# Kernel tuning notes

Hardware: AMD Instinct MI355X
Metric: run time of the kernel (lower is better)

Reference implementation:

```python
import jax, jax.numpy as jnp
import numpy as np

B, H, W, C = 4, 64, 64, 64
GROUPS = 32
EPS = 1e-3  # keras GroupNormalization default


def setup_inputs() -> dict:
    key = jax.random.key(0)
    ks = jax.random.split(key, 6)
    s = 1.0 / np.sqrt(C)
    return {
        'x': jax.random.normal(ks[0], (B, H, W, C), dtype=jnp.float32),
        'gamma': jnp.ones((C,), jnp.float32),
        'beta': jnp.zeros((C,), jnp.float32),
        'wq': jax.random.uniform(ks[1], (C, C), jnp.float32, -s, s),
        'bq': jnp.zeros((C,), jnp.float32),
        'wk': jax.random.uniform(ks[2], (C, C), jnp.float32, -s, s),
        'bk': jnp.zeros((C,), jnp.float32),
        'wv': jax.random.uniform(ks[3], (C, C), jnp.float32, -s, s),
        'bv': jnp.zeros((C,), jnp.float32),
        'wo': jnp.zeros((C, C), jnp.float32),  # init_scale=0.0 -> ~zero init
        'bo': jnp.zeros((C,), jnp.float32),
    }


def group_norm(x, gamma, beta):
    b, h, w, c = x.shape
    xg = x.reshape(b, h, w, GROUPS, c // GROUPS)
    mean = jnp.mean(xg, axis=(1, 2, 4), keepdims=True)
    var = jnp.var(xg, axis=(1, 2, 4), keepdims=True)
    xn = ((xg - mean) * jax.lax.rsqrt(var + EPS)).reshape(b, h, w, c)
    return xn * gamma + beta


def reference(x, gamma, beta, wq, bq, wk, bk, wv, bv, wo, bo):
    b, h, w, c = x.shape
    hn = group_norm(x, gamma, beta)
    # 1x1 convs == per-pixel dense layers
    q = jnp.einsum('bhwc,cd->bhwd', hn, wq) + bq
    k = jnp.einsum('bhwc,cd->bhwd', hn, wk) + bk
    v = jnp.einsum('bhwc,cd->bhwd', hn, wv) + bv
    # full spatial attention scores [B,H,W,H,W]
    scores = jnp.einsum('bhwc,bHWc->bhwHW', q, k) * (float(c) ** -0.5)
    attn = jax.nn.softmax(scores.reshape(b, h, w, h * w), axis=-1)
    attn = attn.reshape(b, h, w, h, w)
    o = jnp.einsum('bhwHW,bHWc->bhwc', attn, v)
    o = jnp.einsum('bhwc,cd->bhwd', o, wo) + bo
    return x + o
```

## Files before the change

kernel.cpp:

```cpp
#include <hip/hip_runtime.h>
#include <math.h>

#define BB 4
#define HH 64
#define WW 64
#define CC 64
#define NN (HH*WW)
#define NPIX (BB*NN)
#define EPS 1e-3f
#define QBLK 32
#define KSPLIT 8
#define NQT32 (NPIX/QBLK)
#define NCHK ((NN/KSPLIT)/64)

using bf16x8 = __attribute__((ext_vector_type(8))) short;
using f32x4  = __attribute__((ext_vector_type(4))) float;
using f32x16 = __attribute__((ext_vector_type(16))) float;

__device__ inline unsigned short bf16bits(float f) {
    union { float f; unsigned u; } a; a.f = f;
    unsigned r = a.u + 0x7fffu + ((a.u >> 16) & 1u);
    return (unsigned short)(r >> 16);
}
__device__ inline unsigned packbf(float lo, float hi) {
    return (unsigned)bf16bits(lo) | ((unsigned)bf16bits(hi) << 16);
}
__device__ inline unsigned cvtpk(float lo, float hi) {
    unsigned r;
    asm("v_cvt_pk_bf16_f32 %0, %1, %2" : "=v"(r) : "v"(lo), "v"(hi));
    return r;
}
#define PSWAP(a, b) asm("v_permlane32_swap_b32 %0, %1" : "+v"(a), "+v"(b))

__device__ __forceinline__ float exp2g(float x) {
    float r;
    asm("v_exp_f32 %0, %1" : "=v"(r) : "v"(x));
    return r;
}

#define QSCALE 0.18033688011112042f

__global__ __launch_bounds__(256) void gn_wt(const float* __restrict__ x,
                                             float* __restrict__ part,
                                             const float* __restrict__ wq,
                                             const float* __restrict__ wk,
                                             const float* __restrict__ wv,
                                             const float* __restrict__ wo,
                                             short* __restrict__ wfrag) {
    int t = threadIdx.x;
    if (blockIdx.x < 256) {
        int c = t & 63, rr = t >> 6;
        int p0 = blockIdx.x * 64;
        float s = 0.f, s2 = 0.f;
        #pragma unroll
        for (int k = 0; k < 16; ++k) {
            float v = x[(size_t)(p0 + rr + 4 * k) * CC + c];
            s += v; s2 += v * v;
        }
        __shared__ float sA[256], sB[256];
        sA[t] = s; sB[t] = s2;
        __syncthreads();
        if (t < 64) {
            float fs  = sA[t] + sA[64 + t] + sA[128 + t] + sA[192 + t];
            float fs2 = sB[t] + sB[64 + t] + sB[128 + t] + sB[192 + t];
            part[blockIdx.x * 128 + t]      = fs;
            part[blockIdx.x * 128 + 64 + t] = fs2;
        }
    } else {
        const float* mats[3] = {wq, wk, wv};
        int i0 = (blockIdx.x - 256) * 256 + t;
        for (int e = i0; e < 12288; e += 16 * 256) {
            int m = e >> 12;
            int r = e & 4095;
            int dt = r >> 10, h = (r >> 9) & 1, lane = (r >> 3) & 63, j = r & 7;
            int g = lane >> 4, cl = lane & 15;
            float v = mats[m][(h * 32 + g * 8 + j) * 64 + dt * 16 + cl];
            wfrag[e] = (short)bf16bits(v);
        }
        for (int e = i0; e < 4096; e += 16 * 256) {
            int j = e & 7, lane = (e >> 3) & 63, dt = (e >> 9) & 1, s = e >> 10;
            int hi = lane >> 5, l31 = lane & 31;
            float v = wo[(8 * hi + 16 * s + j) * 64 + dt * 32 + l31];
            wfrag[12288 + e] = (short)bf16bits(v);
        }
    }
}

__global__ __launch_bounds__(256) void gn_final(const float* __restrict__ part,
                                                const float* __restrict__ gamma,
                                                const float* __restrict__ beta,
                                                float* __restrict__ scale,
                                                float* __restrict__ shift) {
    int b = blockIdx.x;
    int t = threadIdx.x;
    int c = t & 63, rr = t >> 6;
    float s = 0.f, s2 = 0.f;
    #pragma unroll
    for (int k = 0; k < 16; ++k) {
        int blk = b * 64 + rr + 4 * k;
        s  += part[blk * 128 + c];
        s2 += part[blk * 128 + 64 + c];
    }
    __shared__ float sA[256], sB[256];
    sA[t] = s; sB[t] = s2;
    __syncthreads();
    if (t < 64) {
        sA[t] = sA[t] + sA[64 + t] + sA[128 + t] + sA[192 + t];
        sB[t] = sB[t] + sB[64 + t] + sB[128 + t] + sB[192 + t];
    }
    __syncthreads();
    if (t < 64) {
        int g = t >> 1;
        float sumg  = sA[g * 2] + sA[g * 2 + 1];
        float sum2g = sB[g * 2] + sB[g * 2 + 1];
        const float n = (float)(NN * 2);
        float mean = sumg / n;
        float var  = sum2g / n - mean * mean;
        float r = rsqrtf(var + EPS);
        float a = gamma[t] * r;
        scale[b * CC + t] = a;
        shift[b * CC + t] = beta[t] - mean * a;
    }
}

__global__ __launch_bounds__(256) void qkv_proj(
        const float* __restrict__ x,
        const float* __restrict__ scale,
        const float* __restrict__ shift,
        const short* __restrict__ wfrag,
        const float* __restrict__ bq, const float* __restrict__ bk,
        const float* __restrict__ bv,
        short* __restrict__ qb, short* __restrict__ kb,
        short* __restrict__ vt) {
    __shared__ unsigned short vtile[64 * 72];
    int t = threadIdx.x;
    int lane = t & 63, wid = t >> 6;
    int g = lane >> 4, cl = lane & 15;
    int pixblk = blockIdx.x * 64;
    int pix0 = pixblk + wid * 16;
    int b = pixblk >> 12;

    const float* xp = x + (size_t)(pix0 + cl) * CC + g * 8;
    float4 x00 = *(const float4*)(xp);
    float4 x01 = *(const float4*)(xp + 4);
    float4 x10 = *(const float4*)(xp + 32);
    float4 x11 = *(const float4*)(xp + 36);
    const float* scb = scale + b * CC + g * 8;
    const float* sfb = shift + b * CC + g * 8;
    float4 s00 = *(const float4*)(scb);
    float4 s01 = *(const float4*)(scb + 4);
    float4 s10 = *(const float4*)(scb + 32);
    float4 s11 = *(const float4*)(scb + 36);
    float4 f00 = *(const float4*)(sfb);
    float4 f01 = *(const float4*)(sfb + 4);
    float4 f10 = *(const float4*)(sfb + 32);
    float4 f11 = *(const float4*)(sfb + 36);

    union { bf16x8 v; unsigned u[4]; } af0, af1;
    af0.u[0] = packbf(x00.x * s00.x + f00.x, x00.y * s00.y + f00.y);
    af0.u[1] = packbf(x00.z * s00.z + f00.z, x00.w * s00.w + f00.w);
    af0.u[2] = packbf(x01.x * s01.x + f01.x, x01.y * s01.y + f01.y);
    af0.u[3] = packbf(x01.z * s01.z + f01.z, x01.w * s01.w + f01.w);
    af1.u[0] = packbf(x10.x * s10.x + f10.x, x10.y * s10.y + f10.y);
    af1.u[1] = packbf(x10.z * s10.z + f10.z, x10.w * s10.w + f10.w);
    af1.u[2] = packbf(x11.x * s11.x + f11.x, x11.y * s11.y + f11.y);
    af1.u[3] = packbf(x11.z * s11.z + f11.z, x11.w * s11.w + f11.w);

    #pragma unroll
    for (int m = 0; m < 3; ++m) {
        const float* bias = (m == 0) ? bq : (m == 1) ? bk : bv;
        #pragma unroll
        for (int dt = 0; dt < 4; ++dt) {
            bf16x8 w0 = *(const bf16x8*)(wfrag + (size_t)(((m * 4 + dt) * 2 + 0) * 64 + lane) * 8);
            bf16x8 w1 = *(const bf16x8*)(wfrag + (size_t)(((m * 4 + dt) * 2 + 1) * 64 + lane) * 8);
            f32x4 z = (f32x4){0.f, 0.f, 0.f, 0.f};
            z = __builtin_amdgcn_mfma_f32_16x16x32_bf16(af0.v, w0, z, 0, 0, 0);
            z = __builtin_amdgcn_mfma_f32_16x16x32_bf16(af1.v, w1, z, 0, 0, 0);
            float bias_d = bias[dt * 16 + cl];
            if (m == 0) {
                #pragma unroll
                for (int r = 0; r < 4; ++r)
                    qb[(size_t)(pix0 + 4 * g + r) * CC + dt * 16 + cl] =
                        (short)bf16bits((z[r] + bias_d) * QSCALE);
            } else if (m == 1) {
                #pragma unroll
                for (int r = 0; r < 4; ++r)
                    kb[(size_t)(pix0 + 4 * g + r) * CC + dt * 16 + cl] =
                        (short)bf16bits(z[r] + bias_d);
            } else {
                #pragma unroll
                for (int r = 0; r < 4; ++r)
                    vtile[(dt * 16 + cl) * 72 + wid * 16 + 4 * g + r] =
                        bf16bits(z[r] + bias_d);
            }
        }
    }
    __syncthreads();
    {
        int d = t >> 2, seg = t & 3;
        uint4 v0 = *(const uint4*)(vtile + d * 72 + seg * 16);
        uint4 v1 = *(const uint4*)(vtile + d * 72 + seg * 16 + 8);
        uint4* dst = (uint4*)(vt + ((size_t)(b * 64 + d)) * NN + pixblk + seg * 16);
        dst[0] = v0; dst[1] = v1;
    }
}

__global__ __launch_bounds__(256, 2) void attn_mfma64(
        const short* __restrict__ qb, const short* __restrict__ kb,
        const short* __restrict__ vt,
        unsigned* __restrict__ obf, float* __restrict__ msb) {
    __shared__ short lds[2][2][64 * 64];
    const int t = threadIdx.x;
    const int lane = t & 63;
    const int wid  = t >> 6;
    const int hi  = lane >> 5;
    const int l31 = lane & 31;
    const int r7  = l31 & 7;
    const int kseg   = blockIdx.x % KSPLIT;
    const int qblock = blockIdx.x / KSPLIT;
    const int qt0 = (qblock * 4 + wid) * 2;
    const int b = qblock >> 4;
    const int key0 = kseg * (NN / KSPLIT);

    bf16x8 qf[2][4];
    const short* qp = qb + (size_t)(qblock * 256 + wid * 64 + l31) * CC + 8 * hi;
    #pragma unroll
    for (int qc = 0; qc < 2; ++qc)
        #pragma unroll
        for (int s = 0; s < 4; ++s)
            qf[qc][s] = *(const bf16x8*)(qp + qc * 32 * CC + 16 * s);

    const int srow = t >> 3;
    const int scol = t & 7;
    const short* kS = kb + ((size_t)b * NN + key0) * CC;
    const short* vS = vt + ((size_t)b * CC) * NN + key0;

    f32x16 oacc00, oacc01, oacc10, oacc11;
    #pragma unroll
    for (int r = 0; r < 16; ++r) {
        oacc00[r] = 0.f; oacc01[r] = 0.f; oacc10[r] = 0.f; oacc11[r] = 0.f;
    }
    float psum0 = 0.f, psum1 = 0.f;

    auto stage = [&](int ck, int bsel) {
        #pragma unroll
        for (int r = 0; r < 2; ++r) {
            int row = srow + 32 * r;
            const short* src = kS + (size_t)(ck * 64 + row) * CC + (scol ^ (row & 7)) * 8;
            __builtin_amdgcn_global_load_lds(
                (const __attribute__((address_space(1))) void*)src,
                (__attribute__((address_space(3))) void*)&lds[bsel][0][(r * 32 + wid * 8) * 64],
                16, 0, 0);
        }
        #pragma unroll
        for (int r = 0; r < 2; ++r) {
            int row = srow + 32 * r;
            const short* src = vS + (size_t)row * NN + ck * 64 + (scol ^ (row & 7)) * 8;
            __builtin_amdgcn_global_load_lds(
                (const __attribute__((address_space(1))) void*)src,
                (__attribute__((address_space(3))) void*)&lds[bsel][1][(r * 32 + wid * 8) * 64],
                16, 0, 0);
        }
    };

    auto subbody = [&](const short* kB, const short* vB, int ks) {
        bf16x8 kf[4];
        #pragma unroll
        for (int s = 0; s < 4; ++s)
            kf[s] = *(const bf16x8*)(kB + (32 * ks + l31) * 64 + ((2 * s + hi) ^ r7) * 8);
        bf16x8 vf0 = *(const bf16x8*)(vB + (l31) * 64      + ((4 * ks + 0 + hi) ^ r7) * 8);
        bf16x8 vf1 = *(const bf16x8*)(vB + (32 + l31) * 64 + ((4 * ks + 0 + hi) ^ r7) * 8);
        bf16x8 vf2 = *(const bf16x8*)(vB + (l31) * 64      + ((4 * ks + 2 + hi) ^ r7) * 8);
        bf16x8 vf3 = *(const bf16x8*)(vB + (32 + l31) * 64 + ((4 * ks + 2 + hi) ^ r7) * 8);
        {
            f32x16 st;
            #pragma unroll
            for (int r = 0; r < 16; ++r) st[r] = 0.f;
            __builtin_amdgcn_s_setprio(1);
            #pragma unroll
            for (int s = 0; s < 4; ++s)
                st = __builtin_amdgcn_mfma_f32_32x32x16_bf16(kf[s], qf[0][s], st, 0, 0, 0);
            __builtin_amdgcn_s_setprio(0);
            float ps = 0.f;
            #pragma unroll
            for (int r = 0; r < 16; ++r) { st[r] = exp2g(st[r]); ps += st[r]; }
            psum0 += ps;
            unsigned w[8];
            #pragma unroll
            for (int i = 0; i < 8; ++i) w[i] = cvtpk(st[2 * i], st[2 * i + 1]);
            PSWAP(w[0], w[2]); PSWAP(w[1], w[3]);
            PSWAP(w[4], w[6]); PSWAP(w[5], w[7]);
            union { bf16x8 v; unsigned u[4]; } pa0, pa1;
            pa0.u[0] = w[0]; pa0.u[1] = w[1]; pa0.u[2] = w[2]; pa0.u[3] = w[3];
            pa1.u[0] = w[4]; pa1.u[1] = w[5]; pa1.u[2] = w[6]; pa1.u[3] = w[7];
            __builtin_amdgcn_s_setprio(1);
            oacc00 = __builtin_amdgcn_mfma_f32_32x32x16_bf16(pa0.v, vf0, oacc00, 0, 0, 0);
            oacc01 = __builtin_amdgcn_mfma_f32_32x32x16_bf16(pa0.v, vf1, oacc01, 0, 0, 0);
            oacc00 = __builtin_amdgcn_mfma_f32_32x32x16_bf16(pa1.v, vf2, oacc00, 0, 0, 0);
            oacc01 = __builtin_amdgcn_mfma_f32_32x32x16_bf16(pa1.v, vf3, oacc01, 0, 0, 0);
            __builtin_amdgcn_s_setprio(0);
        }
        {
            f32x16 st;
            #pragma unroll
            for (int r = 0; r < 16; ++r) st[r] = 0.f;
            __builtin_amdgcn_s_setprio(1);
            #pragma unroll
            for (int s = 0; s < 4; ++s)
                st = __builtin_amdgcn_mfma_f32_32x32x16_bf16(kf[s], qf[1][s], st, 0, 0, 0);
            __builtin_amdgcn_s_setprio(0);
            float ps = 0.f;
            #pragma unroll
            for (int r = 0; r < 16; ++r) { st[r] = exp2g(st[r]); ps += st[r]; }
            psum1 += ps;
            unsigned w[8];
            #pragma unroll
            for (int i = 0; i < 8; ++i) w[i] = cvtpk(st[2 * i], st[2 * i + 1]);
            PSWAP(w[0], w[2]); PSWAP(w[1], w[3]);
            PSWAP(w[4], w[6]); PSWAP(w[5], w[7]);
            union { bf16x8 v; unsigned u[4]; } pa0, pa1;
            pa0.u[0] = w[0]; pa0.u[1] = w[1]; pa0.u[2] = w[2]; pa0.u[3] = w[3];
            pa1.u[0] = w[4]; pa1.u[1] = w[5]; pa1.u[2] = w[6]; pa1.u[3] = w[7];
            __builtin_amdgcn_s_setprio(1);
            oacc10 = __builtin_amdgcn_mfma_f32_32x32x16_bf16(pa0.v, vf0, oacc10, 0, 0, 0);
            oacc11 = __builtin_amdgcn_mfma_f32_32x32x16_bf16(pa0.v, vf1, oacc11, 0, 0, 0);
            oacc10 = __builtin_amdgcn_mfma_f32_32x32x16_bf16(pa1.v, vf2, oacc10, 0, 0, 0);
            oacc11 = __builtin_amdgcn_mfma_f32_32x32x16_bf16(pa1.v, vf3, oacc11, 0, 0, 0);
            __builtin_amdgcn_s_setprio(0);
        }
    };

    stage(0, 0);
    #pragma unroll 1
    for (int c = 0; c < NCHK; ++c) {
        asm volatile("s_waitcnt vmcnt(0)" ::: "memory");
        __syncthreads();
        if (c + 1 < NCHK) stage(c + 1, (c + 1) & 1);
        const short* kB = &lds[c & 1][0][0];
        const short* vB = &lds[c & 1][1][0];
        subbody(kB, vB, 0);
        subbody(kB, vB, 1);
    }

    {
        int task = (qt0 + 0) * KSPLIT + kseg;
        unsigned* ob32 = obf + (size_t)task * 1024;
        #pragma unroll
        for (int r = 0; r < 16; ++r) {
            int row = (r & 3) + 8 * (r >> 2) + 4 * hi;
            ob32[row * 32 + l31] = cvtpk(oacc00[r], oacc01[r]);
        }
        msb[task * 64 + lane] = psum0;
    }
    {
        int task = (qt0 + 1) * KSPLIT + kseg;
        unsigned* ob32 = obf + (size_t)task * 1024;
        #pragma unroll
        for (int r = 0; r < 16; ++r) {
            int row = (r & 3) + 8 * (r >> 2) + 4 * hi;
            ob32[row * 32 + l31] = cvtpk(oacc10[r], oacc11[r]);
        }
        msb[task * 64 + lane] = psum1;
    }
}

__device__ __forceinline__ void acc2(float& lo_acc, float& hi_acc, unsigned u) {
    union { unsigned u; float f; } a, b;
    a.u = u << 16; b.u = u & 0xffff0000u;
    lo_acc += a.f; hi_acc += b.f;
}

__global__ __launch_bounds__(256) void attn_merge_outproj(
        const unsigned* __restrict__ obf, const float* __restrict__ msb,
        const short* __restrict__ wfrag,
        const float* __restrict__ x,
        const float* __restrict__ bo,
        float* __restrict__ out) {
    int t = threadIdx.x;
    int lane = t & 63, wid = t >> 6;
    int hi = lane >> 5, l31 = lane & 31;
    int qtile = blockIdx.x * 4 + wid;

    float stot = 0.f;
    #pragma unroll
    for (int s = 0; s < KSPLIT; ++s) {
        stot += msb[(qtile * KSPLIT + s) * 64 + l31]
              + msb[(qtile * KSPLIT + s) * 64 + 32 + l31];
    }
    float inv = 1.f / stot;

    float oa[4][8];
    #pragma unroll
    for (int s = 0; s < 4; ++s)
        #pragma unroll
        for (int j = 0; j < 8; ++j) oa[s][j] = 0.f;
    #pragma unroll 4
    for (int ks = 0; ks < KSPLIT; ++ks) {
        const unsigned* base = obf + (size_t)(qtile * KSPLIT + ks) * 1024 + l31 * 32 + 8 * hi;
        uint4 wa = *(const uint4*)(base);
        uint4 wb = *(const uint4*)(base + 4);
        uint4 wc = *(const uint4*)(base + 16);
        uint4 wd = *(const uint4*)(base + 20);
        acc2(oa[0][0], oa[2][0], wa.x); acc2(oa[0][1], oa[2][1], wa.y);
        acc2(oa[0][2], oa[2][2], wa.z); acc2(oa[0][3], oa[2][3], wa.w);
        acc2(oa[0][4], oa[2][4], wb.x); acc2(oa[0][5], oa[2][5], wb.y);
        acc2(oa[0][6], oa[2][6], wb.z); acc2(oa[0][7], oa[2][7], wb.w);
        acc2(oa[1][0], oa[3][0], wc.x); acc2(oa[1][1], oa[3][1], wc.y);
        acc2(oa[1][2], oa[3][2], wc.z); acc2(oa[1][3], oa[3][3], wc.w);
        acc2(oa[1][4], oa[3][4], wd.x); acc2(oa[1][5], oa[3][5], wd.y);
        acc2(oa[1][6], oa[3][6], wd.z); acc2(oa[1][7], oa[3][7], wd.w);
    }
    union { bf16x8 v; unsigned u[4]; } af[4];
    #pragma unroll
    for (int s = 0; s < 4; ++s)
        #pragma unroll
        for (int m = 0; m < 4; ++m)
            af[s].u[m] = cvtpk(oa[s][2 * m] * inv, oa[s][2 * m + 1] * inv);

    const short* w32 = wfrag + 12288;
    f32x16 z0, z1;
    #pragma unroll
    for (int r = 0; r < 16; ++r) { z0[r] = 0.f; z1[r] = 0.f; }
    #pragma unroll
    for (int s = 0; s < 4; ++s) {
        bf16x8 wb0 = *(const bf16x8*)(w32 + (size_t)((s * 2 + 0) * 64 + lane) * 8);
        bf16x8 wb1 = *(const bf16x8*)(w32 + (size_t)((s * 2 + 1) * 64 + lane) * 8);
        z0 = __builtin_amdgcn_mfma_f32_32x32x16_bf16(af[s].v, wb0, z0, 0, 0, 0);
        z1 = __builtin_amdgcn_mfma_f32_32x32x16_bf16(af[s].v, wb1, z1, 0, 0, 0);
    }
    float bo0 = bo[l31], bo1 = bo[32 + l31];
    #pragma unroll
    for (int r = 0; r < 16; ++r) {
        int row = (r & 3) + 8 * (r >> 2) + 4 * hi;
        size_t i0 = (size_t)(qtile * QBLK + row) * CC + l31;
        out[i0]      = x[i0]      + z0[r] + bo0;
        out[i0 + 32] = x[i0 + 32] + z1[r] + bo1;
    }
}

extern "C" void kernel_launch(void* const* d_in, const int* in_sizes, int n_in,
                              void* d_out, int out_size, void* d_ws, size_t ws_size,
                              hipStream_t stream) {
    const float* x     = (const float*)d_in[0];
    const float* gamma = (const float*)d_in[1];
    const float* beta  = (const float*)d_in[2];
    const float* wq    = (const float*)d_in[3];
    const float* bq    = (const float*)d_in[4];
    const float* wk    = (const float*)d_in[5];
    const float* bk    = (const float*)d_in[6];
    const float* wv    = (const float*)d_in[7];
    const float* bv    = (const float*)d_in[8];
    const float* wo    = (const float*)d_in[9];
    const float* bo    = (const float*)d_in[10];
    float* out = (float*)d_out;

    float* ws    = (float*)d_ws;
    float* scale = ws;
    float* shift = scale + 256;
    float* part  = shift + 256;
    short* wfrag = (short*)(part + 32768);
    short* qb    = wfrag + 16384;
    short* kbp   = qb  + (size_t)NPIX * CC;
    short* vtp   = kbp + (size_t)NPIX * CC;
    unsigned* obf = (unsigned*)(vtp + (size_t)NPIX * CC);
    float* msb   = (float*)(obf + (size_t)NQT32 * KSPLIT * 1024);

    hipLaunchKernelGGL(gn_wt, dim3(272), dim3(256), 0, stream,
                       x, part, wq, wk, wv, wo, wfrag);
    hipLaunchKernelGGL(gn_final, dim3(BB), dim3(256), 0, stream,
                       part, gamma, beta, scale, shift);
    hipLaunchKernelGGL(qkv_proj, dim3(256), dim3(256), 0, stream,
                       x, scale, shift, wfrag, bq, bk, bv, qb, kbp, vtp);
    hipLaunchKernelGGL(attn_mfma64, dim3(64 * KSPLIT), dim3(256), 0, stream,
                       qb, kbp, vtp, obf, msb);
    hipLaunchKernelGGL(attn_merge_outproj, dim3(NQT32 / 4), dim3(256), 0, stream,
                       obf, msb, wfrag, x, bo, out);
}
```

Baseline: 47.84 us.

## Fuse group-norm finalize into QKV projection and triple-buffer attention K/V staging

Removes the separate gn_final launch by having every qkv_proj block reduce the group-norm partial sums itself and keep scale/shift in shared memory. The attention kernel goes from double to triple buffering of K/V tiles in LDS, prefetching two chunks ahead. It waits with a partial vmcnt and a bare s_barrier instead of a full drain plus __syncthreads. The setprio hints around the MFMAs are also dropped. The cost is redundant reduction work in each of the 256 qkv blocks and 50% more LDS per attention block, which could lower occupancy.

```diff
diff --git a/kernel.cpp b/kernel.cpp
--- a/kernel.cpp
+++ b/kernel.cpp
@@ -86,53 +86,19 @@
     }
 }
 
-__global__ __launch_bounds__(256) void gn_final(const float* __restrict__ part,
-                                                const float* __restrict__ gamma,
-                                                const float* __restrict__ beta,
-                                                float* __restrict__ scale,
-                                                float* __restrict__ shift) {
-    int b = blockIdx.x;
-    int t = threadIdx.x;
-    int c = t & 63, rr = t >> 6;
-    float s = 0.f, s2 = 0.f;
-    #pragma unroll
-    for (int k = 0; k < 16; ++k) {
-        int blk = b * 64 + rr + 4 * k;
-        s  += part[blk * 128 + c];
-        s2 += part[blk * 128 + 64 + c];
-    }
-    __shared__ float sA[256], sB[256];
-    sA[t] = s; sB[t] = s2;
-    __syncthreads();
-    if (t < 64) {
-        sA[t] = sA[t] + sA[64 + t] + sA[128 + t] + sA[192 + t];
-        sB[t] = sB[t] + sB[64 + t] + sB[128 + t] + sB[192 + t];
-    }
-    __syncthreads();
-    if (t < 64) {
-        int g = t >> 1;
-        float sumg  = sA[g * 2] + sA[g * 2 + 1];
-        float sum2g = sB[g * 2] + sB[g * 2 + 1];
-        const float n = (float)(NN * 2);
-        float mean = sumg / n;
-        float var  = sum2g / n - mean * mean;
-        float r = rsqrtf(var + EPS);
-        float a = gamma[t] * r;
-        scale[b * CC + t] = a;
-        shift[b * CC + t] = beta[t] - mean * a;
-    }
-}
-
 __global__ __launch_bounds__(256) void qkv_proj(
         const float* __restrict__ x,
-        const float* __restrict__ scale,
-        const float* __restrict__ shift,
+        const float* __restrict__ part,
+        const float* __restrict__ gamma,
+        const float* __restrict__ beta,
         const short* __restrict__ wfrag,
         const float* __restrict__ bq, const float* __restrict__ bk,
         const float* __restrict__ bv,
         short* __restrict__ qb, short* __restrict__ kb,
         short* __restrict__ vt) {
     __shared__ unsigned short vtile[64 * 72];
+    __shared__ float sA[256], sB[256];
+    __shared__ float sScale[64], sShift[64];
     int t = threadIdx.x;
     int lane = t & 63, wid = t >> 6;
     int g = lane >> 4, cl = lane & 15;
@@ -140,21 +106,50 @@
     int pix0 = pixblk + wid * 16;
     int b = pixblk >> 12;
 
+    {
+        int c = t & 63, rr = t >> 6;
+        float s = 0.f, s2 = 0.f;
+        #pragma unroll
+        for (int k = 0; k < 16; ++k) {
+            int blk = b * 64 + rr + 4 * k;
+            s  += part[blk * 128 + c];
+            s2 += part[blk * 128 + 64 + c];
+        }
+        sA[t] = s; sB[t] = s2;
+        __syncthreads();
+        if (t < 64) {
+            sA[t] = sA[t] + sA[64 + t] + sA[128 + t] + sA[192 + t];
+            sB[t] = sB[t] + sB[64 + t] + sB[128 + t] + sB[192 + t];
+        }
+        __syncthreads();
+        if (t < 64) {
+            int gg = t >> 1;
+            float sumg  = sA[gg * 2] + sA[gg * 2 + 1];
+            float sum2g = sB[gg * 2] + sB[gg * 2 + 1];
+            const float n = (float)(NN * 2);
+            float mean = sumg / n;
+            float var  = sum2g / n - mean * mean;
+            float r = rsqrtf(var + EPS);
+            float a = gamma[t] * r;
+            sScale[t] = a;
+            sShift[t] = beta[t] - mean * a;
+        }
+        __syncthreads();
+    }
+
     const float* xp = x + (size_t)(pix0 + cl) * CC + g * 8;
     float4 x00 = *(const float4*)(xp);
     float4 x01 = *(const float4*)(xp + 4);
     float4 x10 = *(const float4*)(xp + 32);
     float4 x11 = *(const float4*)(xp + 36);
-    const float* scb = scale + b * CC + g * 8;
-    const float* sfb = shift + b * CC + g * 8;
-    float4 s00 = *(const float4*)(scb);
-    float4 s01 = *(const float4*)(scb + 4);
-    float4 s10 = *(const float4*)(scb + 32);
-    float4 s11 = *(const float4*)(scb + 36);
-    float4 f00 = *(const float4*)(sfb);
-    float4 f01 = *(const float4*)(sfb + 4);
-    float4 f10 = *(const float4*)(sfb + 32);
-    float4 f11 = *(const float4*)(sfb + 36);
+    float4 s00 = *(const float4*)(&sScale[g * 8]);
+    float4 s01 = *(const float4*)(&sScale[g * 8 + 4]);
+    float4 s10 = *(const float4*)(&sScale[g * 8 + 32]);
+    float4 s11 = *(const float4*)(&sScale[g * 8 + 36]);
+    float4 f00 = *(const float4*)(&sShift[g * 8]);
+    float4 f01 = *(const float4*)(&sShift[g * 8 + 4]);
+    float4 f10 = *(const float4*)(&sShift[g * 8 + 32]);
+    float4 f11 = *(const float4*)(&sShift[g * 8 + 36]);
 
     union { bf16x8 v; unsigned u[4]; } af0, af1;
     af0.u[0] = packbf(x00.x * s00.x + f00.x, x00.y * s00.y + f00.y);
@@ -209,7 +204,7 @@
         const short* __restrict__ qb, const short* __restrict__ kb,
         const short* __restrict__ vt,
         unsigned* __restrict__ obf, float* __restrict__ msb) {
-    __shared__ short lds[2][2][64 * 64];
+    __shared__ short lds[3][2][64 * 64];
     const int t = threadIdx.x;
     const int lane = t & 63;
     const int wid  = t >> 6;
@@ -218,7 +213,7 @@
     const int r7  = l31 & 7;
     const int kseg   = blockIdx.x % KSPLIT;
     const int qblock = blockIdx.x / KSPLIT;
-    const int qt0 = (qblock * 4 + wid) * 2;
+    const int qt0 = qblock * 8 + wid * 2;
     const int b = qblock >> 4;
     const int key0 = kseg * (NN / KSPLIT);
 
@@ -276,11 +271,9 @@
             f32x16 st;
             #pragma unroll
             for (int r = 0; r < 16; ++r) st[r] = 0.f;
-            __builtin_amdgcn_s_setprio(1);
             #pragma unroll
             for (int s = 0; s < 4; ++s)
                 st = __builtin_amdgcn_mfma_f32_32x32x16_bf16(kf[s], qf[0][s], st, 0, 0, 0);
-            __builtin_amdgcn_s_setprio(0);
             float ps = 0.f;
             #pragma unroll
             for (int r = 0; r < 16; ++r) { st[r] = exp2g(st[r]); ps += st[r]; }
@@ -293,22 +286,18 @@
             union { bf16x8 v; unsigned u[4]; } pa0, pa1;
             pa0.u[0] = w[0]; pa0.u[1] = w[1]; pa0.u[2] = w[2]; pa0.u[3] = w[3];
             pa1.u[0] = w[4]; pa1.u[1] = w[5]; pa1.u[2] = w[6]; pa1.u[3] = w[7];
-            __builtin_amdgcn_s_setprio(1);
             oacc00 = __builtin_amdgcn_mfma_f32_32x32x16_bf16(pa0.v, vf0, oacc00, 0, 0, 0);
             oacc01 = __builtin_amdgcn_mfma_f32_32x32x16_bf16(pa0.v, vf1, oacc01, 0, 0, 0);
             oacc00 = __builtin_amdgcn_mfma_f32_32x32x16_bf16(pa1.v, vf2, oacc00, 0, 0, 0);
             oacc01 = __builtin_amdgcn_mfma_f32_32x32x16_bf16(pa1.v, vf3, oacc01, 0, 0, 0);
-            __builtin_amdgcn_s_setprio(0);
         }
         {
             f32x16 st;
             #pragma unroll
             for (int r = 0; r < 16; ++r) st[r] = 0.f;
-            __builtin_amdgcn_s_setprio(1);
             #pragma unroll
             for (int s = 0; s < 4; ++s)
                 st = __builtin_amdgcn_mfma_f32_32x32x16_bf16(kf[s], qf[1][s], st, 0, 0, 0);
-            __builtin_amdgcn_s_setprio(0);
             float ps = 0.f;
             #pragma unroll
             for (int r = 0; r < 16; ++r) { st[r] = exp2g(st[r]); ps += st[r]; }
@@ -321,23 +310,31 @@
             union { bf16x8 v; unsigned u[4]; } pa0, pa1;
             pa0.u[0] = w[0]; pa0.u[1] = w[1]; pa0.u[2] = w[2]; pa0.u[3] = w[3];
             pa1.u[0] = w[4]; pa1.u[1] = w[5]; pa1.u[2] = w[6]; pa1.u[3] = w[7];
-            __builtin_amdgcn_s_setprio(1);
             oacc10 = __builtin_amdgcn_mfma_f32_32x32x16_bf16(pa0.v, vf0, oacc10, 0, 0, 0);
             oacc11 = __builtin_amdgcn_mfma_f32_32x32x16_bf16(pa0.v, vf1, oacc11, 0, 0, 0);
             oacc10 = __builtin_amdgcn_mfma_f32_32x32x16_bf16(pa1.v, vf2, oacc10, 0, 0, 0);
             oacc11 = __builtin_amdgcn_mfma_f32_32x32x16_bf16(pa1.v, vf3, oacc11, 0, 0, 0);
-            __builtin_amdgcn_s_setprio(0);
         }
     };
 
     stage(0, 0);
+    stage(1, 1);
     #pragma unroll 1
-    for (int c = 0; c < NCHK; ++c) {
-        asm volatile("s_waitcnt vmcnt(0)" ::: "memory");
-        __syncthreads();
-        if (c + 1 < NCHK) stage(c + 1, (c + 1) & 1);
-        const short* kB = &lds[c & 1][0][0];
-        const short* vB = &lds[c & 1][1][0];
+    for (int c = 0; c < NCHK - 1; ++c) {
+        asm volatile("s_waitcnt vmcnt(4)" ::: "memory");
+        __builtin_amdgcn_s_barrier();
+        if (c + 2 < NCHK) stage(c + 2, (c + 2) % 3);
+        const short* kB = &lds[c % 3][0][0];
+        const short* vB = &lds[c % 3][1][0];
+        subbody(kB, vB, 0);
+        subbody(kB, vB, 1);
+    }
+    asm volatile("s_waitcnt vmcnt(0)" ::: "memory");
+    __builtin_amdgcn_s_barrier();
+    {
+        const int c = NCHK - 1;
+        const short* kB = &lds[c % 3][0][0];
+        const short* vB = &lds[c % 3][1][0];
         subbody(kB, vB, 0);
         subbody(kB, vB, 1);
     }
@@ -455,9 +452,7 @@
     float* out = (float*)d_out;
 
     float* ws    = (float*)d_ws;
-    float* scale = ws;
-    float* shift = scale + 256;
-    float* part  = shift + 256;
+    float* part  = ws;
     short* wfrag = (short*)(part + 32768);
     short* qb    = wfrag + 16384;
     short* kbp   = qb  + (size_t)NPIX * CC;
@@ -467,10 +462,8 @@
 
     hipLaunchKernelGGL(gn_wt, dim3(272), dim3(256), 0, stream,
                        x, part, wq, wk, wv, wo, wfrag);
-    hipLaunchKernelGGL(gn_final, dim3(BB), dim3(256), 0, stream,
-                       part, gamma, beta, scale, shift);
     hipLaunchKernelGGL(qkv_proj, dim3(256), dim3(256), 0, stream,
-                       x, scale, shift, wfrag, bq, bk, bv, qb, kbp, vtp);
+                       x, part, gamma, beta, wfrag, bq, bk, bv, qb, kbp, vtp);
     hipLaunchKernelGGL(attn_mfma64, dim3(64 * KSPLIT), dim3(256), 0, stream,
                        qb, kbp, vtp, obf, msb);
     hipLaunchKernelGGL(attn_merge_outproj, dim3(NQT32 / 4), dim3(256), 0, stream,
```

Measured after the change: 45.61 us. 1.05x faster.
